# Performance work log

Hardware: AMD Instinct MI355X
Metric: run time of the kernel (lower is better)

The kernel has to match this reference:

```python
import jax, jax.numpy as jnp
import numpy as np

D_MODEL = 1024
NUM_HEADS = 16
PERIOD_LEN = 4096
HEAD_DIM = D_MODEL // NUM_HEADS


def setup_inputs() -> dict:
    key = jax.random.key(0)
    ks = jax.random.split(key, 10)
    B, S, D = 2, 2048, D_MODEL
    scale = 1.0 / np.sqrt(D)
    inp = {
        "x": jax.random.normal(ks[0], (B, S, D), dtype=jnp.float32),
        "wq": jax.random.normal(ks[1], (D, D), dtype=jnp.float32) * scale,
        "bq": jnp.zeros((D,), dtype=jnp.float32),
        "wk": jax.random.normal(ks[2], (D, D), dtype=jnp.float32) * scale,
        "bk": jnp.zeros((D,), dtype=jnp.float32),
        "wv": jax.random.normal(ks[3], (D, D), dtype=jnp.float32) * scale,
        "bv": jnp.zeros((D,), dtype=jnp.float32),
        "wo": jax.random.normal(ks[4], (D, D), dtype=jnp.float32) * scale,
        "bo": jnp.zeros((D,), dtype=jnp.float32),
        # original init is zeros; use small randn so bias path is non-trivial
        "rel_bias": jax.random.normal(ks[5], (PERIOD_LEN, NUM_HEADS), dtype=jnp.float32) * 0.02,
    }
    return inp


def reference(x, wq, bq, wk, bk, wv, bv, wo, bo, rel_bias):
    B, S, D = x.shape
    H, Hd = NUM_HEADS, HEAD_DIM
    q = (x @ wq + bq).reshape(B, S, H, Hd).transpose(0, 2, 1, 3)  # [B,H,S,Hd]
    k = (x @ wk + bk).reshape(B, S, H, Hd).transpose(0, 2, 1, 3)
    v = (x @ wv + bv).reshape(B, S, H, Hd).transpose(0, 2, 1, 3)
    scores = jnp.einsum('bhqd,bhkd->bhqk', q, k) / jnp.sqrt(jnp.float32(Hd))
    if S <= PERIOD_LEN:
        pos = jnp.arange(S)
        circ = (pos[:, None] - pos[None, :]) % PERIOD_LEN  # [S,S]
        bias = rel_bias[circ]                               # [S,S,H]
        scores = scores + bias.transpose(2, 0, 1)[None]     # [1,H,S,S]
    attn = jax.nn.softmax(scores, axis=-1)
    out = jnp.einsum('bhqk,bhkd->bhqd', attn, v)
    out = out.transpose(0, 2, 1, 3).reshape(B, S, D)
    return out @ wo + bo
```

## Files before the change

### kernel.cpp

```cpp
#include <hip/hip_runtime.h>
#include <hip/hip_bf16.h>

#define D_MODEL 1024
#define NHEADS  16
#define HEADD   64
#define SEQ     2048
#define PERIOD  4096
#define LOG2E   1.44269504088896340736f

typedef __attribute__((ext_vector_type(4)))  float f32x4;
typedef __attribute__((ext_vector_type(16))) float f32x16;
typedef __attribute__((ext_vector_type(4)))  float fvec4;
typedef __attribute__((ext_vector_type(8)))  short s16x8;
typedef __attribute__((ext_vector_type(4)))  short s16x4;
typedef __attribute__((ext_vector_type(2)))  int   i32x2;
typedef __attribute__((ext_vector_type(4)))  int   i32x4;

__device__ __forceinline__ short bf16_bits(float f) {
    union { float f; unsigned u; } v; v.f = f;
    unsigned r = v.u + 0x7FFFu + ((v.u >> 16) & 1u);
    return (short)(r >> 16);
}

__device__ __forceinline__ int cvt_pk_bf16(float a, float b) {
    int r;
    asm("v_cvt_pk_bf16_f32 %0, %1, %2" : "=v"(r) : "v"(a), "v"(b));
    return r;
}

__device__ __forceinline__ float exp2_hw(float x) {
    float r;
    asm("v_exp_f32 %0, %1" : "=v"(r) : "v"(x));
    return r;
}

__device__ __forceinline__ void gload_lds16(const void* g, void* l) {
    __builtin_amdgcn_global_load_lds(
        (const __attribute__((address_space(1))) void*)g,
        (__attribute__((address_space(3))) void*)l, 16, 0, 0);
}

__global__ void cvt_x(const float* __restrict__ x, short* __restrict__ xb) {
    int i = blockIdx.x * blockDim.x + threadIdx.x;
    fvec4 v = ((const fvec4*)x)[i];
    s16x4 o;
    o.x = bf16_bits(v.x); o.y = bf16_bits(v.y);
    o.z = bf16_bits(v.z); o.w = bf16_bits(v.w);
    ((s16x4*)xb)[i] = o;
}

__global__ void transpose_w(const float* __restrict__ src, short* __restrict__ dst) {
    __shared__ float tile[64][65];
    int bx = blockIdx.x & 15, by = blockIdx.x >> 4;
    int n0 = bx * 64, k0 = by * 64;
    int t = threadIdx.x;
    int cr = t >> 4;
    int cc = (t & 15) * 4;
    for (int i = 0; i < 4; ++i) {
        int row = cr + i * 16;
        fvec4 v = *(const fvec4*)&src[(k0 + row) * D_MODEL + n0 + cc];
        tile[row][cc+0] = v.x; tile[row][cc+1] = v.y;
        tile[row][cc+2] = v.z; tile[row][cc+3] = v.w;
    }
    __syncthreads();
    for (int i = 0; i < 4; ++i) {
        int row = cr + i * 16;
        s16x4 o;
        o.x = bf16_bits(tile[cc+0][row]);
        o.y = bf16_bits(tile[cc+1][row]);
        o.z = bf16_bits(tile[cc+2][row]);
        o.w = bf16_bits(tile[cc+3][row]);
        *(s16x4*)&dst[(n0 + row) * D_MODEL + k0 + cc] = o;
    }
}

__global__ void transpose_v(const short* __restrict__ vb, short* __restrict__ vt) {
    __shared__ short tile[64][80];
    int bh = blockIdx.y, st = blockIdx.x;
    int b = bh >> 4, h = bh & 15;
    int s0 = st * 64;
    int t = threadIdx.x;
    int row = t >> 3, ch = t & 7;
    for (int i = 0; i < 2; ++i) {
        int r = row + i * 32;
        *(s16x8*)&tile[r][ch * 8] =
            *(const s16x8*)&vb[(b * SEQ + s0 + r) * D_MODEL + h * HEADD + ch * 8];
    }
    __syncthreads();
    for (int i = 0; i < 2; ++i) {
        int d = row + i * 32;
        s16x8 o;
        #pragma unroll
        for (int j = 0; j < 8; ++j) o[j] = tile[ch * 8 + j][d];
        *(s16x8*)&vt[(b * D_MODEL + h * HEADD + d) * SEQ + s0 + ch * 8] = o;
    }
}

__global__ void build_biasq(const float* __restrict__ rb, f32x4* __restrict__ bq4) {
    int id = blockIdx.x * 256 + threadIdx.x;
    int h = id >> 12, a = id & 4095;
    f32x4 v;
    #pragma unroll
    for (int j = 0; j < 4; ++j)
        v[j] = rb[((a + j) & (PERIOD - 1)) * NHEADS + h] * LOG2E - 16.0f;
    bq4[id] = v;
}

__global__ __launch_bounds__(256, 3) void gemm_qkv(
    const short* __restrict__ A, const short* __restrict__ Bt,
    const float* __restrict__ biasq, const float* __restrict__ biask,
    const float* __restrict__ biasv,
    short* __restrict__ qb, short* __restrict__ kb, short* __restrict__ vb)
{
    __shared__ short As[2][128 * 64];
    __shared__ short Bs[2][64 * 64];
    int tid = threadIdx.x;
    int lane = tid & 63, wid = tid >> 6;
    int ln = lane & 15, g = lane >> 4;
    int wr = (wid >> 1) * 64, wc = (wid & 1) * 32;

    int bid = blockIdx.x;
    int xcd = bid & 7, slot = bid >> 3;
    int mb = xcd * 4 + (slot / 48);
    int nb = slot % 48;
    int m0 = mb * 128, n0 = nb * 64;

    int wsel = n0 >> 10;
    const float* bias = wsel == 0 ? biasq : (wsel == 1 ? biask : biasv);
    short* dst = wsel == 0 ? qb : (wsel == 1 ? kb : vb);
    float osc = wsel == 0 ? (0.125f * LOG2E) : 1.0f;
    int ncol0 = n0 & 1023;

    f32x4 acc[4][2] = {};

    auto STAGE = [&](int kt, int bi) {
        #pragma unroll
        for (int i = 0; i < 4; ++i) {
            int idx = i * 256 + tid;
            int row = idx >> 3, ch = idx & 7;
            int gch = ch ^ (row & 7);
            gload_lds16(&A[(m0 + row) * 1024 + kt + gch * 8],
                        (char*)&As[bi][0] + (i * 256 + wid * 64) * 16);
        }
        #pragma unroll
        for (int i = 0; i < 2; ++i) {
            int idx = i * 256 + tid;
            int row = idx >> 3, ch = idx & 7;
            int gch = ch ^ (row & 7);
            gload_lds16(&Bt[(n0 + row) * 1024 + kt + gch * 8],
                        (char*)&Bs[bi][0] + (i * 256 + wid * 64) * 16);
        }
    };

    STAGE(0, 0);
    __syncthreads();

    for (int kt = 0; kt < 16; ++kt) {
        int bi = kt & 1;
        if (kt < 15) STAGE((kt + 1) * 64, bi ^ 1);

        s16x8 af[4][2], bfr[2][2];
        #pragma unroll
        for (int m = 0; m < 4; ++m) {
            int row = wr + m * 16 + ln;
            #pragma unroll
            for (int kc = 0; kc < 2; ++kc)
                af[m][kc] = *(const s16x8*)&As[bi][row * 64 + (((kc * 4 + g) ^ (row & 7)) * 8)];
        }
        #pragma unroll
        for (int n = 0; n < 2; ++n) {
            int row = wc + n * 16 + ln;
            #pragma unroll
            for (int kc = 0; kc < 2; ++kc)
                bfr[n][kc] = *(const s16x8*)&Bs[bi][row * 64 + (((kc * 4 + g) ^ (row & 7)) * 8)];
        }
        #pragma unroll
        for (int kc = 0; kc < 2; ++kc)
            #pragma unroll
            for (int m = 0; m < 4; ++m)
                #pragma unroll
                for (int n = 0; n < 2; ++n)
                    acc[m][n] = __builtin_amdgcn_mfma_f32_16x16x32_bf16(af[m][kc], bfr[n][kc], acc[m][n], 0, 0, 0);

        __syncthreads();
    }

    #pragma unroll
    for (int m = 0; m < 4; ++m) {
        int gr0 = m0 + wr + m * 16 + g * 4;
        #pragma unroll
        for (int n = 0; n < 2; ++n) {
            int gc = ncol0 + wc + n * 16 + ln;
            float bvv = bias[gc];
            #pragma unroll
            for (int r = 0; r < 4; ++r)
                dst[(gr0 + r) * 1024 + gc] = bf16_bits((acc[m][n][r] + bvv) * osc);
        }
    }
}

template<int MODE>
__global__ __launch_bounds__(256) void gemm_bias(
    const short* __restrict__ A, const short* __restrict__ Bt,
    const float* __restrict__ bias, void* __restrict__ Cout)
{
    __shared__ short As[2][128 * 64];
    __shared__ short Bs[2][64 * 64];
    int tid = threadIdx.x;
    int lane = tid & 63, wid = tid >> 6;
    int ln = lane & 15, g = lane >> 4;
    int wr = (wid >> 1) * 64, wc = (wid & 1) * 32;

    int bid = blockIdx.x;
    int xcd = bid & 7, slot = bid >> 3;
    int mb = xcd * 4 + (slot >> 4);
    int nb = slot & 15;
    int m0 = mb * 128, n0 = nb * 64;

    f32x4 acc[4][2] = {};

    auto STAGE = [&](int kt, int bi) {
        #pragma unroll
        for (int i = 0; i < 4; ++i) {
            int idx = i * 256 + tid;
            int row = idx >> 3, ch = idx & 7;
            int gch = ch ^ (row & 7);
            gload_lds16(&A[(m0 + row) * 1024 + kt + gch * 8],
                        (char*)&As[bi][0] + (i * 256 + wid * 64) * 16);
        }
        #pragma unroll
        for (int i = 0; i < 2; ++i) {
            int idx = i * 256 + tid;
            int row = idx >> 3, ch = idx & 7;
            int gch = ch ^ (row & 7);
            gload_lds16(&Bt[(n0 + row) * 1024 + kt + gch * 8],
                        (char*)&Bs[bi][0] + (i * 256 + wid * 64) * 16);
        }
    };

    STAGE(0, 0);
    __syncthreads();

    for (int kt = 0; kt < 16; ++kt) {
        int bi = kt & 1;
        if (kt < 15) STAGE((kt + 1) * 64, bi ^ 1);

        s16x8 af[4][2], bfr[2][2];
        #pragma unroll
        for (int m = 0; m < 4; ++m) {
            int row = wr + m * 16 + ln;
            #pragma unroll
            for (int kc = 0; kc < 2; ++kc)
                af[m][kc] = *(const s16x8*)&As[bi][row * 64 + (((kc * 4 + g) ^ (row & 7)) * 8)];
        }
        #pragma unroll
        for (int n = 0; n < 2; ++n) {
            int row = wc + n * 16 + ln;
            #pragma unroll
            for (int kc = 0; kc < 2; ++kc)
                bfr[n][kc] = *(const s16x8*)&Bs[bi][row * 64 + (((kc * 4 + g) ^ (row & 7)) * 8)];
        }
        #pragma unroll
        for (int kc = 0; kc < 2; ++kc)
            #pragma unroll
            for (int m = 0; m < 4; ++m)
                #pragma unroll
                for (int n = 0; n < 2; ++n)
                    acc[m][n] = __builtin_amdgcn_mfma_f32_16x16x32_bf16(af[m][kc], bfr[n][kc], acc[m][n], 0, 0, 0);

        __syncthreads();
    }

    #pragma unroll
    for (int m = 0; m < 4; ++m) {
        int gr0 = m0 + wr + m * 16 + g * 4;
        #pragma unroll
        for (int n = 0; n < 2; ++n) {
            int gc = n0 + wc + n * 16 + ln;
            float bv = bias[gc];
            #pragma unroll
            for (int r = 0; r < 4; ++r) {
                int gr = gr0 + r;
                float v = acc[m][n][r] + bv;
                if (MODE == 0)      ((short*)Cout)[gr * 1024 + gc] = bf16_bits(v * (0.125f * LOG2E));
                else if (MODE == 1) ((short*)Cout)[gr * 1024 + gc] = bf16_bits(v);
                else                ((float*)Cout)[gr * 1024 + gc] = v;
            }
        }
    }
}

__global__ __launch_bounds__(512, 2) void attn_kernel(
    const short* __restrict__ qb,
    const short* __restrict__ kb,
    const short* __restrict__ vt,
    const f32x4* __restrict__ biasq,
    short* __restrict__ ao)
{
    __shared__ short KV[2][2][2][64 * 64];

    int tid = threadIdx.x;
    int half = tid >> 8;
    int tid_h = tid & 255;
    int lane = tid & 63;
    int wid_h = (tid >> 6) & 3;
    int l31 = lane & 31, hi = lane >> 5;

    int bid = blockIdx.x;
    int xcd = bid & 7, slot = bid >> 3;
    int hb = xcd * 4 + (slot >> 4);
    int qt = slot & 15;
    int h = hb & 15, b = hb >> 4;
    int q0 = qt * 128 + wid_h * 32;
    int qrow = q0 + l31;
    int kbase = half * 1024;

    s16x8 aq[4];
    #pragma unroll
    for (int kk = 0; kk < 4; ++kk)
        aq[kk] = *(const s16x8*)&qb[(b * SEQ + qrow) * D_MODEL + h * HEADD + kk * 16 + hi * 8];

    const f32x4* bq = biasq + h * PERIOD;

    float lrow = 0.f;
    f32x16 ot[2] = {};

    auto STAGE = [&](int k0, int bi) {
        #pragma unroll
        for (int i = 0; i < 2; ++i) {
            int idx = i * 256 + tid_h;
            int row = idx >> 3, ch = idx & 7;
            int gch = ch ^ ((row & 7) ^ ((row >> 3) & 3));
            gload_lds16(&kb[(b * SEQ + k0 + row) * D_MODEL + h * HEADD + gch * 8],
                        (char*)&KV[half][bi][0][0] + (i * 256 + wid_h * 64) * 16);
            gload_lds16(&vt[(b * D_MODEL + h * HEADD + row) * SEQ + k0 + gch * 8],
                        (char*)&KV[half][bi][1][0] + (i * 256 + wid_h * 64) * 16);
        }
    };

    STAGE(kbase, 0);
    __syncthreads();

    for (int kt = 0; kt < 16; ++kt) {
        int k0 = kbase + kt * 64;
        int bi = kt & 1;
        if (kt < 15) STAGE(k0 + 64, bi ^ 1);

        f32x4 bv[2][4];
        #pragma unroll
        for (int kt32 = 0; kt32 < 2; ++kt32)
            #pragma unroll
            for (int rq = 0; rq < 4; ++rq) {
                int kq = k0 + kt32 * 32 + rq * 8 + hi * 4;
                bv[kt32][rq] = bq[(qrow - kq - 3) & (PERIOD - 1)];
            }

        f32x16 s[2];
        const short* Ksp = &KV[half][bi][0][0];
        const short* Vsp = &KV[half][bi][1][0];
        __builtin_amdgcn_s_setprio(1);
        #pragma unroll
        for (int kt32 = 0; kt32 < 2; ++kt32) {
            f32x16 acc = {};
            int rowK = kt32 * 32 + l31;
            int swz = (rowK & 7) ^ ((rowK >> 3) & 3);
            #pragma unroll
            for (int kk = 0; kk < 4; ++kk) {
                s16x8 kf = *(const s16x8*)&Ksp[rowK * 64 + (((2 * kk + hi) ^ swz) * 8)];
                acc = __builtin_amdgcn_mfma_f32_32x32x16_bf16(kf, aq[kk], acc, 0, 0, 0);
            }
            s[kt32] = acc;
        }
        __builtin_amdgcn_s_setprio(0);

        #pragma unroll
        for (int kt32 = 0; kt32 < 2; ++kt32)
            #pragma unroll
            for (int rq = 0; rq < 4; ++rq) {
                s[kt32][rq * 4 + 0] = exp2_hw(s[kt32][rq * 4 + 0] + bv[kt32][rq][3]);
                s[kt32][rq * 4 + 1] = exp2_hw(s[kt32][rq * 4 + 1] + bv[kt32][rq][2]);
                s[kt32][rq * 4 + 2] = exp2_hw(s[kt32][rq * 4 + 2] + bv[kt32][rq][1]);
                s[kt32][rq * 4 + 3] = exp2_hw(s[kt32][rq * 4 + 3] + bv[kt32][rq][0]);
            }

        float sm[16];
        #pragma unroll
        for (int t = 0; t < 16; ++t) sm[t] = s[0][t] + s[1][t];
        #pragma unroll
        for (int t = 0; t < 8; ++t) sm[t] += sm[t + 8];
        #pragma unroll
        for (int t = 0; t < 4; ++t) sm[t] += sm[t + 4];
        float psum = (sm[0] + sm[1]) + (sm[2] + sm[3]);
        {
            i32x2 r = __builtin_amdgcn_permlane32_swap(__float_as_int(psum), __float_as_int(psum), false, false);
            psum = __int_as_float(r[0]) + __int_as_float(r[1]);
        }
        lrow += psum;

        #pragma unroll
        for (int kt32 = 0; kt32 < 2; ++kt32) {
            int pk[8];
            #pragma unroll
            for (int i = 0; i < 8; ++i)
                pk[i] = cvt_pk_bf16(s[kt32][2 * i], s[kt32][2 * i + 1]);
            #pragma unroll
            for (int ks = 0; ks < 2; ++ks) {
                int a0 = pk[ks * 4 + 0], b0 = pk[ks * 4 + 2];
                int a1 = pk[ks * 4 + 1], b1 = pk[ks * 4 + 3];
                int a0s = __shfl_xor(a0, 32), b0s = __shfl_xor(b0, 32);
                int a1s = __shfl_xor(a1, 32), b1s = __shfl_xor(b1, 32);
                i32x4 wi;
                wi[0] = (lane < 32) ? a0 : b0s;
                wi[1] = (lane < 32) ? a1 : b1s;
                wi[2] = (lane < 32) ? a0s : b0;
                wi[3] = (lane < 32) ? a1s : b1;
                s16x8 pb = __builtin_bit_cast(s16x8, wi);
                __builtin_amdgcn_s_setprio(1);
                #pragma unroll
                for (int dd = 0; dd < 2; ++dd) {
                    int rowV = dd * 32 + l31;
                    int swzV = (rowV & 7) ^ ((rowV >> 3) & 3);
                    int chV = kt32 * 4 + ks * 2 + hi;
                    s16x8 vf = *(const s16x8*)&Vsp[rowV * 64 + ((chV ^ swzV) * 8)];
                    ot[dd] = __builtin_amdgcn_mfma_f32_32x32x16_bf16(vf, pb, ot[dd], 0, 0, 0);
                }
                __builtin_amdgcn_s_setprio(0);
            }
        }

        __syncthreads();
    }

    float* mbuf = (float*)&KV[0][0][0][0];
    float* slot_p = mbuf + (wid_h * 64 + lane) * 33;
    if (half == 1) {
        #pragma unroll
        for (int dd = 0; dd < 2; ++dd)
            #pragma unroll
            for (int t = 0; t < 16; ++t)
                slot_p[dd * 16 + t] = ot[dd][t];
        slot_p[32] = lrow;
    }
    __syncthreads();
    if (half == 0) {
        lrow += slot_p[32];
        float inv = 1.0f / lrow;
        int obase = (b * SEQ + qrow) * D_MODEL + h * HEADD;
        #pragma unroll
        for (int dd = 0; dd < 2; ++dd)
            #pragma unroll
            for (int rq = 0; rq < 4; ++rq) {
                float v0 = (ot[dd][rq * 4 + 0] + slot_p[dd * 16 + rq * 4 + 0]) * inv;
                float v1 = (ot[dd][rq * 4 + 1] + slot_p[dd * 16 + rq * 4 + 1]) * inv;
                float v2 = (ot[dd][rq * 4 + 2] + slot_p[dd * 16 + rq * 4 + 2]) * inv;
                float v3 = (ot[dd][rq * 4 + 3] + slot_p[dd * 16 + rq * 4 + 3]) * inv;
                i32x2 st;
                st[0] = cvt_pk_bf16(v0, v1);
                st[1] = cvt_pk_bf16(v2, v3);
                *(i32x2*)&ao[obase + dd * 32 + rq * 8 + hi * 4] = st;
            }
    }
}

extern "C" void kernel_launch(void* const* d_in, const int* in_sizes, int n_in,
                              void* d_out, int out_size, void* d_ws, size_t ws_size,
                              hipStream_t stream) {
    const float* x  = (const float*)d_in[0];
    const float* wq = (const float*)d_in[1];
    const float* bq = (const float*)d_in[2];
    const float* wk = (const float*)d_in[3];
    const float* bk = (const float*)d_in[4];
    const float* wv = (const float*)d_in[5];
    const float* bv = (const float*)d_in[6];
    const float* wo = (const float*)d_in[7];
    const float* bo = (const float*)d_in[8];
    const float* rb = (const float*)d_in[9];

    char* ws = (char*)d_ws;
    short* xb  = (short*)(ws);
    short* wqt = (short*)(ws + (8u  << 20));
    short* wkt = (short*)(ws + (10u << 20));
    short* wvt = (short*)(ws + (12u << 20));
    short* wot = (short*)(ws + (14u << 20));
    short* qb  = (short*)(ws + (16u << 20));
    short* kb  = (short*)(ws + (24u << 20));
    short* vb  = (short*)(ws + (32u << 20));
    short* vt  = (short*)(ws + (40u << 20));
    f32x4* bqt = (f32x4*)(ws + (32u << 20));
    short* ao  = xb;

    cvt_x<<<4096, 256, 0, stream>>>(x, xb);
    transpose_w<<<256, 256, 0, stream>>>(wq, wqt);
    transpose_w<<<256, 256, 0, stream>>>(wk, wkt);
    transpose_w<<<256, 256, 0, stream>>>(wv, wvt);
    transpose_w<<<256, 256, 0, stream>>>(wo, wot);

    gemm_qkv<<<1536, 256, 0, stream>>>(xb, wqt, bq, bk, bv, qb, kb, vb);
    transpose_v<<<dim3(32, 32), 256, 0, stream>>>(vb, vt);
    build_biasq<<<256, 256, 0, stream>>>(rb, bqt);

    attn_kernel<<<512, 512, 0, stream>>>(qb, kb, vt, bqt, ao);

    gemm_bias<3><<<512, 256, 0, stream>>>(ao, wot, bo, (float*)d_out);
}
```

Before: 143.2 us.

## Split attention KV halves into separate blocks with global partial merge kernel

The attention kernel previously ran both KV halves inside one 512-thread block and merged them through LDS. Each half now runs as its own 256-thread block (1024 blocks, 4 per CU by launch bounds). The blocks write fp32 partial outputs and row sums to workspace, and a separate merge kernel normalizes them and converts to bf16. The four weight-transpose launches are also fused into one 2D-grid launch. The split gives finer scheduling granularity and smaller blocks, at the cost of about 32MB of extra fp32 global traffic and one more kernel launch.

```diff
diff --git a/kernel.cpp b/kernel.cpp
--- a/kernel.cpp
+++ b/kernel.cpp
@@ -49,8 +49,13 @@
     ((s16x4*)xb)[i] = o;
 }
 
-__global__ void transpose_w(const float* __restrict__ src, short* __restrict__ dst) {
+__global__ void transpose_w4(const float* __restrict__ wq, const float* __restrict__ wk,
+                             const float* __restrict__ wv, const float* __restrict__ wo,
+                             short* __restrict__ wqkv, short* __restrict__ wot) {
     __shared__ float tile[64][65];
+    int wsel = blockIdx.y;
+    const float* src = wsel == 0 ? wq : (wsel == 1 ? wk : (wsel == 2 ? wv : wo));
+    short* dst = wsel < 3 ? wqkv + wsel * 1024 * 1024 : wot;
     int bx = blockIdx.x & 15, by = blockIdx.x >> 4;
     int n0 = bx * 64, k0 = by * 64;
     int t = threadIdx.x;
@@ -290,28 +295,28 @@
     }
 }
 
-__global__ __launch_bounds__(512, 2) void attn_kernel(
+__global__ __launch_bounds__(256, 4) void attn_partial(
     const short* __restrict__ qb,
     const short* __restrict__ kb,
     const short* __restrict__ vt,
     const f32x4* __restrict__ biasq,
-    short* __restrict__ ao)
+    float* __restrict__ po,
+    float* __restrict__ pl)
 {
-    __shared__ short KV[2][2][2][64 * 64];
+    __shared__ short KV[2][2][64 * 64];
 
     int tid = threadIdx.x;
-    int half = tid >> 8;
-    int tid_h = tid & 255;
     int lane = tid & 63;
-    int wid_h = (tid >> 6) & 3;
+    int wid = tid >> 6;
     int l31 = lane & 31, hi = lane >> 5;
 
     int bid = blockIdx.x;
     int xcd = bid & 7, slot = bid >> 3;
-    int hb = xcd * 4 + (slot >> 4);
-    int qt = slot & 15;
+    int hb = xcd * 4 + (slot >> 5);
+    int qt = (slot >> 1) & 15;
+    int half = slot & 1;
     int h = hb & 15, b = hb >> 4;
-    int q0 = qt * 128 + wid_h * 32;
+    int q0 = qt * 128 + wid * 32;
     int qrow = q0 + l31;
     int kbase = half * 1024;
 
@@ -328,13 +333,13 @@
     auto STAGE = [&](int k0, int bi) {
         #pragma unroll
         for (int i = 0; i < 2; ++i) {
-            int idx = i * 256 + tid_h;
+            int idx = i * 256 + tid;
             int row = idx >> 3, ch = idx & 7;
             int gch = ch ^ ((row & 7) ^ ((row >> 3) & 3));
             gload_lds16(&kb[(b * SEQ + k0 + row) * D_MODEL + h * HEADD + gch * 8],
-                        (char*)&KV[half][bi][0][0] + (i * 256 + wid_h * 64) * 16);
+                        (char*)&KV[bi][0][0] + (i * 256 + wid * 64) * 16);
             gload_lds16(&vt[(b * D_MODEL + h * HEADD + row) * SEQ + k0 + gch * 8],
-                        (char*)&KV[half][bi][1][0] + (i * 256 + wid_h * 64) * 16);
+                        (char*)&KV[bi][1][0] + (i * 256 + wid * 64) * 16);
         }
     };
 
@@ -356,8 +361,8 @@
             }
 
         f32x16 s[2];
-        const short* Ksp = &KV[half][bi][0][0];
-        const short* Vsp = &KV[half][bi][1][0];
+        const short* Ksp = &KV[bi][0][0];
+        const short* Vsp = &KV[bi][1][0];
         __builtin_amdgcn_s_setprio(1);
         #pragma unroll
         for (int kt32 = 0; kt32 < 2; ++kt32) {
@@ -431,35 +436,44 @@
         __syncthreads();
     }
 
-    float* mbuf = (float*)&KV[0][0][0][0];
-    float* slot_p = mbuf + (wid_h * 64 + lane) * 33;
-    if (half == 1) {
-        #pragma unroll
-        for (int dd = 0; dd < 2; ++dd)
-            #pragma unroll
-            for (int t = 0; t < 16; ++t)
-                slot_p[dd * 16 + t] = ot[dd][t];
-        slot_p[32] = lrow;
-    }
-    __syncthreads();
-    if (half == 0) {
-        lrow += slot_p[32];
-        float inv = 1.0f / lrow;
-        int obase = (b * SEQ + qrow) * D_MODEL + h * HEADD;
-        #pragma unroll
-        for (int dd = 0; dd < 2; ++dd)
-            #pragma unroll
-            for (int rq = 0; rq < 4; ++rq) {
-                float v0 = (ot[dd][rq * 4 + 0] + slot_p[dd * 16 + rq * 4 + 0]) * inv;
-                float v1 = (ot[dd][rq * 4 + 1] + slot_p[dd * 16 + rq * 4 + 1]) * inv;
-                float v2 = (ot[dd][rq * 4 + 2] + slot_p[dd * 16 + rq * 4 + 2]) * inv;
-                float v3 = (ot[dd][rq * 4 + 3] + slot_p[dd * 16 + rq * 4 + 3]) * inv;
-                i32x2 st;
-                st[0] = cvt_pk_bf16(v0, v1);
-                st[1] = cvt_pk_bf16(v2, v3);
-                *(i32x2*)&ao[obase + dd * 32 + rq * 8 + hi * 4] = st;
-            }
-    }
+    float* poH = po + half * (4096 * 1024);
+    int obase = (b * SEQ + qrow) * D_MODEL + h * HEADD;
+    #pragma unroll
+    for (int dd = 0; dd < 2; ++dd)
+        #pragma unroll
+        for (int rq = 0; rq < 4; ++rq) {
+            f32x4 st;
+            st[0] = ot[dd][rq * 4 + 0];
+            st[1] = ot[dd][rq * 4 + 1];
+            st[2] = ot[dd][rq * 4 + 2];
+            st[3] = ot[dd][rq * 4 + 3];
+            *(f32x4*)&poH[obase + dd * 32 + rq * 8 + hi * 4] = st;
+        }
+    if (hi == 0)
+        pl[half * (4096 * 16) + (b * SEQ + qrow) * 16 + h] = lrow;
+}
+
+__global__ __launch_bounds__(256) void attn_merge(
+    const float* __restrict__ po, const float* __restrict__ pl,
+    short* __restrict__ ao)
+{
+    int idx = blockIdx.x * 256 + threadIdx.x;
+    int base = idx * 8;
+    int row = base >> 10, col = base & 1023, h = col >> 6;
+    float l = pl[row * 16 + h] + pl[4096 * 16 + row * 16 + h];
+    float inv = 1.0f / l;
+    const float* p0 = po + row * 1024 + col;
+    const float* p1 = p0 + 4096 * 1024;
+    f32x4 a0 = *(const f32x4*)p0;
+    f32x4 a1 = *(const f32x4*)(p0 + 4);
+    f32x4 b0 = *(const f32x4*)p1;
+    f32x4 b1 = *(const f32x4*)(p1 + 4);
+    i32x4 o;
+    o[0] = cvt_pk_bf16((a0[0] + b0[0]) * inv, (a0[1] + b0[1]) * inv);
+    o[1] = cvt_pk_bf16((a0[2] + b0[2]) * inv, (a0[3] + b0[3]) * inv);
+    o[2] = cvt_pk_bf16((a1[0] + b1[0]) * inv, (a1[1] + b1[1]) * inv);
+    o[3] = cvt_pk_bf16((a1[2] + b1[2]) * inv, (a1[3] + b1[3]) * inv);
+    *(i32x4*)&ao[base] = o;
 }
 
 extern "C" void kernel_launch(void* const* d_in, const int* in_sizes, int n_in,
@@ -477,29 +491,27 @@
     const float* rb = (const float*)d_in[9];
 
     char* ws = (char*)d_ws;
-    short* xb  = (short*)(ws);
-    short* wqt = (short*)(ws + (8u  << 20));
-    short* wkt = (short*)(ws + (10u << 20));
-    short* wvt = (short*)(ws + (12u << 20));
-    short* wot = (short*)(ws + (14u << 20));
-    short* qb  = (short*)(ws + (16u << 20));
-    short* kb  = (short*)(ws + (24u << 20));
-    short* vb  = (short*)(ws + (32u << 20));
-    short* vt  = (short*)(ws + (40u << 20));
-    f32x4* bqt = (f32x4*)(ws + (32u << 20));
-    short* ao  = xb;
+    short* xb   = (short*)(ws);
+    short* wqkv = (short*)(ws + (8u  << 20));
+    short* wot  = (short*)(ws + (14u << 20));
+    short* qb   = (short*)(ws + (16u << 20));
+    short* kb   = (short*)(ws + (24u << 20));
+    short* vb   = (short*)(ws + (32u << 20));
+    short* vt   = (short*)(ws + (40u << 20));
+    f32x4* bqt  = (f32x4*)(ws + (32u << 20));
+    float* po   = (float*)(ws + (48u << 20));
+    float* pl   = (float*)(ws + (80u << 20));
+    short* ao   = xb;
 
     cvt_x<<<4096, 256, 0, stream>>>(x, xb);
-    transpose_w<<<256, 256, 0, stream>>>(wq, wqt);
-    transpose_w<<<256, 256, 0, stream>>>(wk, wkt);
-    transpose_w<<<256, 256, 0, stream>>>(wv, wvt);
-    transpose_w<<<256, 256, 0, stream>>>(wo, wot);
-
-    gemm_qkv<<<1536, 256, 0, stream>>>(xb, wqt, bq, bk, bv, qb, kb, vb);
+    transpose_w4<<<dim3(256, 4), 256, 0, stream>>>(wq, wk, wv, wo, wqkv, wot);
+
+    gemm_qkv<<<1536, 256, 0, stream>>>(xb, wqkv, bq, bk, bv, qb, kb, vb);
     transpose_v<<<dim3(32, 32), 256, 0, stream>>>(vb, vt);
     build_biasq<<<256, 256, 0, stream>>>(rb, bqt);
 
-    attn_kernel<<<512, 512, 0, stream>>>(qb, kb, vt, bqt, ao);
+    attn_partial<<<1024, 256, 0, stream>>>(qb, kb, vt, bqt, po, pl);
+    attn_merge<<<2048, 256, 0, stream>>>(po, pl, ao);
 
     gemm_bias<3><<<512, 256, 0, stream>>>(ao, wot, bo, (float*)d_out);
 }
```

Measured after the change: 149.3 us. 1.04x slower.
